# Kernel tuning notes

Measured on AMD Instinct MI355X. Metric: run time of the kernel, lower is better.

## Reference

```python
import jax, jax.numpy as jnp
import numpy as np

DIM = 64
N_NEIGHBOR = 32
N_ENTITY = 1_000_000
N_RELATION = 64
N_USER = 500_000
BATCH = 16384


def _xavier_uniform(key, shape):
    fan_in, fan_out = shape[0], shape[1]
    bound = float(np.sqrt(6.0 / (fan_in + fan_out)))
    return jax.random.uniform(key, shape, jnp.float32, -bound, bound)


def setup_inputs() -> dict:
    key = jax.random.key(0)
    ks = jax.random.split(key, 10)
    users = jax.random.randint(ks[0], (BATCH,), 0, N_USER)
    items = jax.random.randint(ks[1], (BATCH,), 0, N_ENTITY)
    label = jnp.round(jax.random.uniform(ks[2], (BATCH,), jnp.float32))
    neighbor_rel = jax.random.randint(ks[3], (BATCH, N_NEIGHBOR), 0, N_RELATION)
    neighbor_tail = jax.random.randint(ks[4], (BATCH, N_NEIGHBOR), 0, N_ENTITY)
    user_emb = _xavier_uniform(ks[5], (N_USER, DIM))
    entity_emb = _xavier_uniform(ks[6], (N_ENTITY, DIM))
    relation_emb = _xavier_uniform(ks[7], (N_RELATION, DIM))
    in_dim = 2 * N_NEIGHBOR * DIM
    wb = float(np.sqrt(1.0 / in_dim))  # torch Linear default init bound
    gen_W = jax.random.uniform(ks[8], (DIM, in_dim), jnp.float32, -wb, wb)
    gen_b = jax.random.uniform(ks[9], (DIM,), jnp.float32, -wb, wb)
    return {"users": users, "items": items, "label": label,
            "neighbor_rel": neighbor_rel, "neighbor_tail": neighbor_tail,
            "user_emb": user_emb, "entity_emb": entity_emb,
            "relation_emb": relation_emb, "gen_W": gen_W, "gen_b": gen_b}


def _bce(p, y):
    # torch BCELoss: clamps log terms at -100, mean reduction
    logp = jnp.clip(jnp.log(p), -100.0)
    log1mp = jnp.clip(jnp.log1p(-p), -100.0)
    return -jnp.mean(y * logp + (1.0 - y) * log1mp)


def reference(users, items, label, neighbor_rel, neighbor_tail,
              user_emb, entity_emb, relation_emb, gen_W, gen_b):
    u = user_emb[users]                       # [B, D]
    i = entity_emb[items]                     # [B, D]
    predict = jax.nn.sigmoid(jnp.sum(u * i, axis=1))

    rel = relation_emb[neighbor_rel]          # [B, K, D]
    tail = entity_emb[neighbor_tail]          # [B, K, D]
    t_r = jnp.concatenate([rel, tail], axis=-1).reshape(u.shape[0], -1)  # [B, 2*K*D]
    false_item = jax.nn.sigmoid(t_r @ gen_W.T + gen_b)                   # [B, D]
    false_predict = jax.nn.sigmoid(jnp.sum(u * false_item, axis=1))

    return _bce(predict, label) + _bce(false_predict, label)
```

## Files before the change

kernel.cpp:

```cpp
#include <hip/hip_runtime.h>
#include <hip/hip_bf16.h>

#define BATCH 16384
#define DIM   64
#define NNB   32
#define INDIM 4096
#define BR    32
#define NBLK  (BATCH / BR)

typedef __attribute__((ext_vector_type(8))) short          s16x8;
typedef __attribute__((ext_vector_type(4))) float          f32x4;
typedef __attribute__((ext_vector_type(4))) unsigned short u16x4;

__device__ __forceinline__ float bf2f(unsigned short u) {
    union { unsigned int i; float f; } v;
    v.i = ((unsigned int)u) << 16;
    return v.f;
}

template<bool FP32>
__device__ __forceinline__ float ldT(const void* p, size_t i) {
    if constexpr (FP32) return ((const float*)p)[i];
    else                return bf2f(((const unsigned short*)p)[i]);
}

template<bool FP32>
__device__ __forceinline__ f32x4 ld4(const void* p, size_t i) {
    if constexpr (FP32) {
        return *(const f32x4*)((const float*)p + i);
    } else {
        const u16x4 v = *(const u16x4*)((const unsigned short*)p + i);
        f32x4 r;
        #pragma unroll
        for (int j = 0; j < 4; ++j) r[j] = bf2f(v[j]);
        return r;
    }
}

__device__ __forceinline__ void split8(const f32x4 x, const f32x4 y, s16x8& h, s16x8& l) {
    #pragma unroll
    for (int j = 0; j < 8; ++j) {
        const float v = (j < 4) ? x[j] : y[j - 4];
        union { float f; unsigned u; } a, b, c;
        a.f = v;
        const unsigned short hh = (unsigned short)(a.u >> 16);
        b.u = ((unsigned)hh) << 16;
        c.f = v - b.f;
        h[j] = (short)hh;
        l[j] = (short)(c.u >> 16);
    }
}

__global__ void kgnn_probe(const unsigned int* __restrict__ lab, int* __restrict__ flag) {
    if (threadIdx.x == 0) {
        int ok = 1;
        for (int i = 0; i < 32; ++i) {
            unsigned int w = lab[i];
            if (!(w == 0u || w == 0x3F800000u)) ok = 0;
        }
        *flag = ok;
    }
}

template<bool FP32>
__global__ __launch_bounds__(512, 4) void kgnn_gemm(
    const int* __restrict__ users, const int* __restrict__ items,
    const void* __restrict__ label_, const int* __restrict__ nrel,
    const int* __restrict__ ntail,  const void* __restrict__ uemb_,
    const void* __restrict__ eemb_, const void* __restrict__ remb_,
    const void* __restrict__ W_,    const void* __restrict__ b_,
    double* __restrict__ acc, double* __restrict__ bsum,
    const int* __restrict__ flag, const int force)
{
    if (force < 0 && *flag != (FP32 ? 1 : 0)) return;

    __shared__ int   sidx[2][BR][NNB + 1];
    __shared__ float fl[2][BR][DIM];
    __shared__ float st[BR];

    const int t    = threadIdx.x;
    const int base = blockIdx.x * BR;
    const int lane = t & 63;
    const int w    = t >> 6;
    const int r16  = lane & 15;
    const int kg   = lane >> 4;
    const int dt   = w & 3;
    const int kh   = w >> 2;

    #pragma unroll
    for (int it = 0; it < 2; ++it) {
        const int e = it * 512 + t;
        const int row = e >> 5, n = e & 31;
        sidx[0][row][n] = nrel [(size_t)base * NNB + e];
        sidx[1][row][n] = ntail[(size_t)base * NNB + e];
    }
    __syncthreads();

    f32x4 ac[2] = { {0.f,0.f,0.f,0.f}, {0.f,0.f,0.f,0.f} };
    const int dcol = dt * 16 + r16;

    if constexpr (!FP32) {
        const unsigned short* E  = (const unsigned short*)eemb_;
        const unsigned short* R  = (const unsigned short*)remb_;
        const unsigned short* wb = (const unsigned short*)W_ + (size_t)dcol * INDIM + kg * 8;
        #pragma unroll 2
        for (int nn = 0; nn < NNB / 2; ++nn) {
            const int n = kh * (NNB / 2) + nn;
            const unsigned short* wn = wb + n * 128;
            const s16x8 b0 = *(const s16x8*)(wn);
            const s16x8 b1 = *(const s16x8*)(wn + 32);
            const s16x8 b2 = *(const s16x8*)(wn + 64);
            const s16x8 b3 = *(const s16x8*)(wn + 96);
            #pragma unroll
            for (int rt = 0; rt < 2; ++rt) {
                const int ri = sidx[0][rt * 16 + r16][n];
                const int ti = sidx[1][rt * 16 + r16][n];
                const unsigned short* rr = R + (size_t)ri * DIM + kg * 8;
                const unsigned short* tr = E + (size_t)ti * DIM + kg * 8;
                const s16x8 a0 = *(const s16x8*)(rr);
                const s16x8 a1 = *(const s16x8*)(rr + 32);
                const s16x8 a2 = *(const s16x8*)(tr);
                const s16x8 a3 = *(const s16x8*)(tr + 32);
                ac[rt] = __builtin_amdgcn_mfma_f32_16x16x32_bf16(a0, b0, ac[rt], 0, 0, 0);
                ac[rt] = __builtin_amdgcn_mfma_f32_16x16x32_bf16(a1, b1, ac[rt], 0, 0, 0);
                ac[rt] = __builtin_amdgcn_mfma_f32_16x16x32_bf16(a2, b2, ac[rt], 0, 0, 0);
                ac[rt] = __builtin_amdgcn_mfma_f32_16x16x32_bf16(a3, b3, ac[rt], 0, 0, 0);
            }
        }
    } else {
        const float* E  = (const float*)eemb_;
        const float* R  = (const float*)remb_;
        const float* wb = (const float*)W_ + (size_t)dcol * INDIM + kg * 8;
        for (int nn = 0; nn < NNB / 2; ++nn) {
            const int n = kh * (NNB / 2) + nn;
            const float* wn = wb + n * 128;
            s16x8 bh[4], bl[4];
            #pragma unroll
            for (int s = 0; s < 4; ++s)
                split8(*(const f32x4*)(wn + s * 32), *(const f32x4*)(wn + s * 32 + 4),
                       bh[s], bl[s]);
            #pragma unroll
            for (int rt = 0; rt < 2; ++rt) {
                const int ri = sidx[0][rt * 16 + r16][n];
                const int ti = sidx[1][rt * 16 + r16][n];
                const float* rr = R + (size_t)ri * DIM + kg * 8;
                const float* tr = E + (size_t)ti * DIM + kg * 8;
                #pragma unroll
                for (int s = 0; s < 4; ++s) {
                    const float* ap = (s < 2) ? rr + s * 32 : tr + (s - 2) * 32;
                    s16x8 ah, al;
                    split8(*(const f32x4*)(ap), *(const f32x4*)(ap + 4), ah, al);
                    ac[rt] = __builtin_amdgcn_mfma_f32_16x16x32_bf16(ah, bh[s], ac[rt], 0, 0, 0);
                    ac[rt] = __builtin_amdgcn_mfma_f32_16x16x32_bf16(ah, bl[s], ac[rt], 0, 0, 0);
                    ac[rt] = __builtin_amdgcn_mfma_f32_16x16x32_bf16(al, bh[s], ac[rt], 0, 0, 0);
                }
            }
        }
    }

    #pragma unroll
    for (int rt = 0; rt < 2; ++rt) {
        #pragma unroll
        for (int q = 0; q < 4; ++q)
            fl[kh][rt * 16 + kg * 4 + q][dcol] = ac[rt][q];
    }
    __syncthreads();

    {
        const int row  = t >> 4;
        const int c    = t & 15;
        const int grow = base + row;
        const int uid  = users[grow], iid = items[grow];
        const f32x4 uv = ld4<FP32>(uemb_, (size_t)uid * DIM + c * 4);
        const f32x4 iv = ld4<FP32>(eemb_, (size_t)iid * DIM + c * 4);
        const f32x4 bv = ld4<FP32>(b_, (size_t)c * 4);
        float p1 = 0.f, p2 = 0.f;
        #pragma unroll
        for (int j = 0; j < 4; ++j) {
            const float lg = fl[0][row][c * 4 + j] + fl[1][row][c * 4 + j] + bv[j];
            const float fi = 1.f / (1.f + expf(-lg));
            p2 += uv[j] * fi;
            p1 += uv[j] * iv[j];
        }
        #pragma unroll
        for (int m = 1; m < 16; m <<= 1) {
            p1 += __shfl_xor(p1, m, 16);
            p2 += __shfl_xor(p2, m, 16);
        }
        if (c == 0) {
            const float y  = ldT<FP32>(label_, grow);
            const float pa = 1.f / (1.f + expf(-p1));
            const float pb = 1.f / (1.f + expf(-p2));
            st[row] =
                  y * fmaxf(logf(pa), -100.f) + (1.f - y) * fmaxf(log1pf(-pa), -100.f)
                + y * fmaxf(logf(pb), -100.f) + (1.f - y) * fmaxf(log1pf(-pb), -100.f);
        }
    }
    __syncthreads();

    if (t < 64) {
        float s = (t < BR) ? st[t] : 0.f;
        #pragma unroll
        for (int m = 1; m < 64; m <<= 1) s += __shfl_xor(s, m, 64);
        if (t == 0) {
            if (bsum) bsum[blockIdx.x] = (double)s;
            else      atomicAdd(acc, (double)s);
        }
    }
}

__global__ void kgnn_fin(const double* __restrict__ acc, const double* __restrict__ bsum,
                         const int* __restrict__ flag, void* __restrict__ out,
                         const int mode) {
    __shared__ double sd[4];
    const int t = threadIdx.x;
    double s = 0.0;
    if (bsum) {
        for (int i = t; i < NBLK; i += 256) s += bsum[i];
    } else if (t == 0) {
        s = *acc;
    }
    #pragma unroll
    for (int m = 1; m < 64; m <<= 1) s += __shfl_xor(s, m, 64);
    if ((t & 63) == 0) sd[t >> 6] = s;
    __syncthreads();
    if (t == 0) {
        const double tot = sd[0] + sd[1] + sd[2] + sd[3];
        const int md = (mode < 0) ? *flag : mode;
        const float loss = (float)(-tot / (double)BATCH);
        if (md) ((float*)out)[0] = loss;
        else    ((__hip_bfloat16*)out)[0] = __float2bfloat16(loss);
    }
}

extern "C" void kernel_launch(void* const* d_in, const int* in_sizes, int n_in,
                              void* d_out, int out_size, void* d_ws, size_t ws_size,
                              hipStream_t stream) {
    const int* users = (const int*)d_in[0];
    const int* items = (const int*)d_in[1];
    const void* label = d_in[2];
    const int* nrel  = (const int*)d_in[3];
    const int* ntail = (const int*)d_in[4];
    const void* uemb = d_in[5];
    const void* eemb = d_in[6];
    const void* remb = d_in[7];
    const void* genW = d_in[8];
    const void* genb = d_in[9];

    double* acc  = (double*)d_ws;
    int*    flag = (int*)((char*)d_ws + 8);
    double* bsum = (ws_size >= (size_t)(16 + NBLK * 8))
                       ? (double*)((char*)d_ws + 16) : nullptr;
    hipMemsetAsync(d_ws, 0, 16, stream);

    const bool f32sz  = (out_size == 4) && (in_sizes[5] == 128000000);
    const bool bf16sz = (out_size == 2) && (in_sizes[5] == 64000000);

    if (f32sz) {
        kgnn_gemm<true><<<NBLK, 512, 0, stream>>>(
            users, items, label, nrel, ntail, uemb, eemb, remb, genW, genb,
            acc, bsum, flag, 1);
        kgnn_fin<<<1, 256, 0, stream>>>(acc, bsum, flag, d_out, 1);
    } else if (bf16sz) {
        kgnn_gemm<false><<<NBLK, 512, 0, stream>>>(
            users, items, label, nrel, ntail, uemb, eemb, remb, genW, genb,
            acc, bsum, flag, 0);
        kgnn_fin<<<1, 256, 0, stream>>>(acc, bsum, flag, d_out, 0);
    } else {
        kgnn_probe<<<1, 64, 0, stream>>>((const unsigned int*)label, flag);
        kgnn_gemm<false><<<NBLK, 512, 0, stream>>>(
            users, items, label, nrel, ntail, uemb, eemb, remb, genW, genb,
            acc, bsum, flag, -1);
        kgnn_gemm<true><<<NBLK, 512, 0, stream>>>(
            users, items, label, nrel, ntail, uemb, eemb, remb, genW, genb,
            acc, bsum, flag, -1);
        kgnn_fin<<<1, 256, 0, stream>>>(acc, bsum, flag, d_out, -1);
    }
}
```

Before: 522.0 us.

## Split neighbors across waves so each gathered row feeds all output dims

The GEMM block now handles 16 batch rows with 4 waves, and each wave owns a slice of 8 neighbors. Each wave computes all 64 output columns, so every gathered relation and entity row is loaded once and reused across four dim tiles. Before, each of four dim-tile waves re-gathered the same rows. Neighbor indices now arrive in registers and are broadcast with wave shuffles instead of being staged through shared memory, and the four partial sums are reduced in shared memory. In exchange, each wave loads four times more weight data per neighbor, which relies on the small weight matrix staying in cache, and register pressure rises from the four accumulators.

```diff
diff --git a/kernel.cpp b/kernel.cpp
--- a/kernel.cpp
+++ b/kernel.cpp
@@ -5,7 +5,9 @@
 #define DIM   64
 #define NNB   32
 #define INDIM 4096
-#define BR    32
+#define BR    16
+#define WPB   4
+#define NPW   (NNB / WPB)
 #define NBLK  (BATCH / BR)
 
 typedef __attribute__((ext_vector_type(8))) short          s16x8;
@@ -63,7 +65,7 @@
 }
 
 template<bool FP32>
-__global__ __launch_bounds__(512, 4) void kgnn_gemm(
+__global__ __launch_bounds__(256, 4) void kgnn_gemm(
     const int* __restrict__ users, const int* __restrict__ items,
     const void* __restrict__ label_, const int* __restrict__ nrel,
     const int* __restrict__ ntail,  const void* __restrict__ uemb_,
@@ -74,8 +76,7 @@
 {
     if (force < 0 && *flag != (FP32 ? 1 : 0)) return;
 
-    __shared__ int   sidx[2][BR][NNB + 1];
-    __shared__ float fl[2][BR][DIM];
+    __shared__ float fl[WPB][BR][68];
     __shared__ float st[BR];
 
     const int t    = threadIdx.x;
@@ -84,86 +85,87 @@
     const int w    = t >> 6;
     const int r16  = lane & 15;
     const int kg   = lane >> 4;
-    const int dt   = w & 3;
-    const int kh   = w >> 2;
-
-    #pragma unroll
-    for (int it = 0; it < 2; ++it) {
-        const int e = it * 512 + t;
-        const int row = e >> 5, n = e & 31;
-        sidx[0][row][n] = nrel [(size_t)base * NNB + e];
-        sidx[1][row][n] = ntail[(size_t)base * NNB + e];
-    }
-    __syncthreads();
-
-    f32x4 ac[2] = { {0.f,0.f,0.f,0.f}, {0.f,0.f,0.f,0.f} };
-    const int dcol = dt * 16 + r16;
+    const int n0   = w * NPW;
+
+    int pr0, pr1, pt0, pt1;
+    {
+        const size_t rb = (size_t)(base + r16) * NNB + n0;
+        pr0 = nrel [rb + kg];
+        pr1 = nrel [rb + 4 + kg];
+        pt0 = ntail[rb + kg];
+        pt1 = ntail[rb + 4 + kg];
+    }
+
+    f32x4 ac[4] = { {0,0,0,0}, {0,0,0,0}, {0,0,0,0}, {0,0,0,0} };
 
     if constexpr (!FP32) {
-        const unsigned short* E  = (const unsigned short*)eemb_;
-        const unsigned short* R  = (const unsigned short*)remb_;
-        const unsigned short* wb = (const unsigned short*)W_ + (size_t)dcol * INDIM + kg * 8;
+        const unsigned short* E = (const unsigned short*)eemb_;
+        const unsigned short* R = (const unsigned short*)remb_;
+        const unsigned short* W = (const unsigned short*)W_;
         #pragma unroll 2
-        for (int nn = 0; nn < NNB / 2; ++nn) {
-            const int n = kh * (NNB / 2) + nn;
-            const unsigned short* wn = wb + n * 128;
-            const s16x8 b0 = *(const s16x8*)(wn);
-            const s16x8 b1 = *(const s16x8*)(wn + 32);
-            const s16x8 b2 = *(const s16x8*)(wn + 64);
-            const s16x8 b3 = *(const s16x8*)(wn + 96);
+        for (int q = 0; q < NPW; ++q) {
+            const int n    = n0 + q;
+            const int ridx = __shfl((q & 4) ? pr1 : pr0, r16 + 16 * (q & 3), 64);
+            const int tidx = __shfl((q & 4) ? pt1 : pt0, r16 + 16 * (q & 3), 64);
+            const unsigned short* rr = R + (size_t)ridx * DIM + kg * 8;
+            const unsigned short* tr = E + (size_t)tidx * DIM + kg * 8;
+            const s16x8 a0 = *(const s16x8*)(rr);
+            const s16x8 a1 = *(const s16x8*)(rr + 32);
+            const s16x8 a2 = *(const s16x8*)(tr);
+            const s16x8 a3 = *(const s16x8*)(tr + 32);
+            const unsigned short* wq = W + (size_t)r16 * INDIM + n * 128 + kg * 8;
             #pragma unroll
-            for (int rt = 0; rt < 2; ++rt) {
-                const int ri = sidx[0][rt * 16 + r16][n];
-                const int ti = sidx[1][rt * 16 + r16][n];
-                const unsigned short* rr = R + (size_t)ri * DIM + kg * 8;
-                const unsigned short* tr = E + (size_t)ti * DIM + kg * 8;
-                const s16x8 a0 = *(const s16x8*)(rr);
-                const s16x8 a1 = *(const s16x8*)(rr + 32);
-                const s16x8 a2 = *(const s16x8*)(tr);
-                const s16x8 a3 = *(const s16x8*)(tr + 32);
-                ac[rt] = __builtin_amdgcn_mfma_f32_16x16x32_bf16(a0, b0, ac[rt], 0, 0, 0);
-                ac[rt] = __builtin_amdgcn_mfma_f32_16x16x32_bf16(a1, b1, ac[rt], 0, 0, 0);
-                ac[rt] = __builtin_amdgcn_mfma_f32_16x16x32_bf16(a2, b2, ac[rt], 0, 0, 0);
-                ac[rt] = __builtin_amdgcn_mfma_f32_16x16x32_bf16(a3, b3, ac[rt], 0, 0, 0);
+            for (int dt = 0; dt < 4; ++dt) {
+                const unsigned short* wd = wq + (size_t)dt * 16 * INDIM;
+                const s16x8 b0 = *(const s16x8*)(wd);
+                const s16x8 b1 = *(const s16x8*)(wd + 32);
+                const s16x8 b2 = *(const s16x8*)(wd + 64);
+                const s16x8 b3 = *(const s16x8*)(wd + 96);
+                ac[dt] = __builtin_amdgcn_mfma_f32_16x16x32_bf16(a0, b0, ac[dt], 0, 0, 0);
+                ac[dt] = __builtin_amdgcn_mfma_f32_16x16x32_bf16(a1, b1, ac[dt], 0, 0, 0);
+                ac[dt] = __builtin_amdgcn_mfma_f32_16x16x32_bf16(a2, b2, ac[dt], 0, 0, 0);
+                ac[dt] = __builtin_amdgcn_mfma_f32_16x16x32_bf16(a3, b3, ac[dt], 0, 0, 0);
             }
         }
     } else {
-        const float* E  = (const float*)eemb_;
-        const float* R  = (const float*)remb_;
-        const float* wb = (const float*)W_ + (size_t)dcol * INDIM + kg * 8;
-        for (int nn = 0; nn < NNB / 2; ++nn) {
-            const int n = kh * (NNB / 2) + nn;
-            const float* wn = wb + n * 128;
-            s16x8 bh[4], bl[4];
+        const float* E = (const float*)eemb_;
+        const float* R = (const float*)remb_;
+        const float* W = (const float*)W_;
+        #pragma unroll 2
+        for (int q = 0; q < NPW; ++q) {
+            const int n    = n0 + q;
+            const int ridx = __shfl((q & 4) ? pr1 : pr0, r16 + 16 * (q & 3), 64);
+            const int tidx = __shfl((q & 4) ? pt1 : pt0, r16 + 16 * (q & 3), 64);
+            const float* rr = R + (size_t)ridx * DIM + kg * 8;
+            const float* tr = E + (size_t)tidx * DIM + kg * 8;
+            s16x8 ah[4], al[4];
             #pragma unroll
-            for (int s = 0; s < 4; ++s)
-                split8(*(const f32x4*)(wn + s * 32), *(const f32x4*)(wn + s * 32 + 4),
-                       bh[s], bl[s]);
+            for (int s = 0; s < 4; ++s) {
+                const float* ap = (s < 2) ? rr + s * 32 : tr + (s - 2) * 32;
+                split8(*(const f32x4*)(ap), *(const f32x4*)(ap + 4), ah[s], al[s]);
+            }
+            const float* wq = W + (size_t)r16 * INDIM + n * 128 + kg * 8;
             #pragma unroll
-            for (int rt = 0; rt < 2; ++rt) {
-                const int ri = sidx[0][rt * 16 + r16][n];
-                const int ti = sidx[1][rt * 16 + r16][n];
-                const float* rr = R + (size_t)ri * DIM + kg * 8;
-                const float* tr = E + (size_t)ti * DIM + kg * 8;
+            for (int dt = 0; dt < 4; ++dt) {
+                const float* wd = wq + (size_t)dt * 16 * INDIM;
                 #pragma unroll
                 for (int s = 0; s < 4; ++s) {
-                    const float* ap = (s < 2) ? rr + s * 32 : tr + (s - 2) * 32;
-                    s16x8 ah, al;
-                    split8(*(const f32x4*)(ap), *(const f32x4*)(ap + 4), ah, al);
-                    ac[rt] = __builtin_amdgcn_mfma_f32_16x16x32_bf16(ah, bh[s], ac[rt], 0, 0, 0);
-                    ac[rt] = __builtin_amdgcn_mfma_f32_16x16x32_bf16(ah, bl[s], ac[rt], 0, 0, 0);
-                    ac[rt] = __builtin_amdgcn_mfma_f32_16x16x32_bf16(al, bh[s], ac[rt], 0, 0, 0);
+                    s16x8 bh, bl;
+                    split8(*(const f32x4*)(wd + s * 32), *(const f32x4*)(wd + s * 32 + 4),
+                           bh, bl);
+                    ac[dt] = __builtin_amdgcn_mfma_f32_16x16x32_bf16(ah[s], bh, ac[dt], 0, 0, 0);
+                    ac[dt] = __builtin_amdgcn_mfma_f32_16x16x32_bf16(ah[s], bl, ac[dt], 0, 0, 0);
+                    ac[dt] = __builtin_amdgcn_mfma_f32_16x16x32_bf16(al[s], bh, ac[dt], 0, 0, 0);
                 }
             }
         }
     }
 
     #pragma unroll
-    for (int rt = 0; rt < 2; ++rt) {
-        #pragma unroll
-        for (int q = 0; q < 4; ++q)
-            fl[kh][rt * 16 + kg * 4 + q][dcol] = ac[rt][q];
-    }
+    for (int dt = 0; dt < 4; ++dt)
+        #pragma unroll
+        for (int qq = 0; qq < 4; ++qq)
+            fl[w][kg * 4 + qq][dt * 16 + r16] = ac[dt][qq];
     __syncthreads();
 
     {
@@ -177,7 +179,9 @@
         float p1 = 0.f, p2 = 0.f;
         #pragma unroll
         for (int j = 0; j < 4; ++j) {
-            const float lg = fl[0][row][c * 4 + j] + fl[1][row][c * 4 + j] + bv[j];
+            const int d = c * 4 + j;
+            const float lg = fl[0][row][d] + fl[1][row][d]
+                           + fl[2][row][d] + fl[3][row][d] + bv[j];
             const float fi = 1.f / (1.f + expf(-lg));
             p2 += uv[j] * fi;
             p1 += uv[j] * iv[j];
@@ -257,21 +261,21 @@
     const bool bf16sz = (out_size == 2) && (in_sizes[5] == 64000000);
 
     if (f32sz) {
-        kgnn_gemm<true><<<NBLK, 512, 0, stream>>>(
+        kgnn_gemm<true><<<NBLK, 256, 0, stream>>>(
             users, items, label, nrel, ntail, uemb, eemb, remb, genW, genb,
             acc, bsum, flag, 1);
         kgnn_fin<<<1, 256, 0, stream>>>(acc, bsum, flag, d_out, 1);
     } else if (bf16sz) {
-        kgnn_gemm<false><<<NBLK, 512, 0, stream>>>(
+        kgnn_gemm<false><<<NBLK, 256, 0, stream>>>(
             users, items, label, nrel, ntail, uemb, eemb, remb, genW, genb,
             acc, bsum, flag, 0);
         kgnn_fin<<<1, 256, 0, stream>>>(acc, bsum, flag, d_out, 0);
     } else {
         kgnn_probe<<<1, 64, 0, stream>>>((const unsigned int*)label, flag);
-        kgnn_gemm<false><<<NBLK, 512, 0, stream>>>(
+        kgnn_gemm<false><<<NBLK, 256, 0, stream>>>(
             users, items, label, nrel, ntail, uemb, eemb, remb, genW, genb,
             acc, bsum, flag, -1);
-        kgnn_gemm<true><<<NBLK, 512, 0, stream>>>(
+        kgnn_gemm<true><<<NBLK, 256, 0, stream>>>(
             users, items, label, nrel, ntail, uemb, eemb, remb, genW, genb,
             acc, bsum, flag, -1);
         kgnn_fin<<<1, 256, 0, stream>>>(acc, bsum, flag, d_out, -1);
```

New measurement: 509.9 us. -2.3%, faster.
